# Kernel tuning notes

Measured on AMD Instinct MI355X. Metric: run time of the kernel, lower is better.

## Reference

```python
import jax, jax.numpy as jnp
import numpy as np

DIM = 1024
G = 256            # group_size
QK = 128           # query_key_dim
HID = 2048         # int(dim * expansion_factor)
NUM_BUCKETS = 32
MAX_DIST = 128
BIAS_SCALE = QK ** 0.5
LN_EPS = 1e-5


def t5_rel_bias(rel_table):
    # causal T5 relative position bias for a [G, G] block
    pos = jnp.arange(G)
    rel = pos[None, :] - pos[:, None]          # k_pos - q_pos
    n = jnp.maximum(-rel, 0)                   # causal clamp
    max_exact = NUM_BUCKETS // 2               # 16
    is_small = n < max_exact
    ln_ratio = np.log(MAX_DIST / max_exact)
    val_large = max_exact + (
        jnp.log(jnp.maximum(n, 1).astype(jnp.float32) / max_exact) / ln_ratio
        * (NUM_BUCKETS - max_exact)
    ).astype(jnp.int32)
    val_large = jnp.minimum(val_large, NUM_BUCKETS - 1)
    bucket = jnp.where(is_small, n, val_large)
    return rel_table[bucket] * BIAS_SCALE      # [G, G]


def setup_inputs() -> dict:
    key = jax.random.key(0)
    ks = jax.random.split(key, 10)
    s = 0.02
    return {
        "x": jax.random.normal(ks[0], (4, 4096, DIM), dtype=jnp.float32),
        "ln_w": jnp.ones((DIM,), jnp.float32),
        "ln_b": jnp.zeros((DIM,), jnp.float32),
        "Wh": jax.random.normal(ks[1], (DIM, 2 * HID), jnp.float32) * s,
        "bh": jnp.zeros((2 * HID,), jnp.float32),
        "Wqk": jax.random.normal(ks[2], (DIM, QK), jnp.float32) * s,
        "bqk": jnp.zeros((QK,), jnp.float32),
        "qk_w": jax.random.normal(ks[3], (4, QK), jnp.float32) * s + 1.0,
        "qk_b": jnp.zeros((4, QK), jnp.float32),
        "rel_table": jax.random.normal(ks[4], (NUM_BUCKETS,), jnp.float32) * s,
        "Wout": jax.random.normal(ks[5], (HID, DIM), jnp.float32) * s,
        "bout": jnp.zeros((DIM,), jnp.float32),
    }


def reference(x, ln_w, ln_b, Wh, bh, Wqk, bqk, qk_w, qk_b, rel_table, Wout, bout):
    b, n, _ = x.shape
    g = G
    ng = n // g

    # LayerNorm
    mu = jnp.mean(x, -1, keepdims=True)
    var = jnp.var(x, -1, keepdims=True)
    normed = (x - mu) * jax.lax.rsqrt(var + LN_EPS) * ln_w + ln_b

    # projections
    hv = jax.nn.silu(normed @ Wh + bh)
    v, gate = jnp.split(hv, 2, axis=-1)                 # [b, n, HID] each
    qk = jax.nn.silu(normed @ Wqk + bqk)                # [b, n, QK]

    # offset-scale into 4 heads
    qk4 = qk[..., None, :] * qk_w + qk_b                # [b, n, 4, QK]
    quad_q, lin_q, quad_k, lin_k = [qk4[..., h, :] for h in range(4)]

    # group: b (g n) d -> b g n d
    grp = lambda t: t.reshape(b, ng, g, t.shape[-1])
    quad_q, quad_k, lin_q, lin_k, vg = map(grp, (quad_q, quad_k, lin_q, lin_k, v))

    # quadratic branch: ReLU^2 attention with T5 bias, causal within group
    sim = jnp.einsum('bgid,bgjd->bgij', quad_q, quad_k) / g
    sim = sim + t5_rel_bias(rel_table)
    attn = jnp.square(jax.nn.relu(sim))
    causal_mask = jnp.triu(jnp.ones((g, g), bool), 1)
    attn = jnp.where(causal_mask, 0.0, attn)
    quad_out = jnp.einsum('bgij,bgje->bgie', attn, vg)  # [b, ng, g, HID]

    # linear branch: per-group kv summary, causal via shifted cumsum over groups
    lin_kv = jnp.einsum('bgnd,bgne->bgde', lin_k, vg) / g   # [b, ng, QK, HID]
    lin_kv = jnp.cumsum(lin_kv, axis=1)
    lin_kv = jnp.pad(lin_kv, ((0, 0), (1, 0), (0, 0), (0, 0)))[:, :-1]
    lin_out = jnp.einsum('bgde,bgnd->bgne', lin_kv, lin_q)  # [b, ng, g, HID]

    out = gate * (quad_out + lin_out).reshape(b, n, HID)
    return out @ Wout + bout + x
```

## Files before the change

### kernel.cpp

```cpp
#include <hip/hip_runtime.h>
#include <hip/hip_bf16.h>

typedef unsigned short u16;
typedef short s8v __attribute__((ext_vector_type(8)));
typedef float f4v __attribute__((ext_vector_type(4)));

__device__ __forceinline__ float b2f(u16 u) { return __uint_as_float(((unsigned)u) << 16); }
__device__ __forceinline__ u16 f2b(float f) {
    unsigned u = __float_as_uint(f);
    unsigned r = 0x7FFFu + ((u >> 16) & 1u);
    return (u16)((u + r) >> 16);
}
__device__ __forceinline__ float silu_f(float x) { return x / (1.0f + expf(-x)); }

__device__ __forceinline__ void gld16(const u16* g, u16* l) {
    __builtin_amdgcn_global_load_lds((const __attribute__((address_space(1))) unsigned*)g,
                                     (__attribute__((address_space(3))) unsigned*)l, 16, 0, 0);
}

__device__ __forceinline__ void mfma_block(const u16* Al, const u16* Bl, f4v acc[4][4],
                                           int wr, int wc, int l15, int quad, int l7) {
#pragma unroll
    for (int ks = 0; ks < 2; ++ks) {
        s8v af[4], bf[4];
        int cch = ((ks * 4 + quad) ^ l7) * 8;
#pragma unroll
        for (int mi = 0; mi < 4; ++mi)
            af[mi] = *(const s8v*)(Al + (wr * 64 + mi * 16 + l15) * 64 + cch);
#pragma unroll
        for (int ni = 0; ni < 4; ++ni)
            bf[ni] = *(const s8v*)(Bl + (wc * 64 + ni * 16 + l15) * 64 + cch);
#pragma unroll
        for (int mi = 0; mi < 4; ++mi)
#pragma unroll
            for (int ni = 0; ni < 4; ++ni)
                acc[mi][ni] = __builtin_amdgcn_mfma_f32_16x16x32_bf16(af[mi], bf[ni], acc[mi][ni], 0, 0, 0);
    }
}


__device__ __forceinline__ void stage_half(const u16* __restrict__ src, int K, int kbase,
                                           u16* dst, int t) {
    const int row = t >> 2, ch = t & 3;
    const int csw = (ch ^ (row & 3) ^ ((row >> 2) & 3)) * 8;
    gld16(src + (size_t)row * K + kbase + csw, dst + row * 32 + ch * 8);
    gld16(src + (size_t)(row + 128) * K + kbase + csw, dst + (row + 128) * 32 + ch * 8);
}

__device__ __forceinline__ void readA4(const u16* Ab, s8v af[4], int rbase, int l15, int quad) {
#pragma unroll
    for (int mi = 0; mi < 4; ++mi) {
        int ra = rbase + mi * 16 + l15;
        af[mi] = *(const s8v*)(Ab + ra * 32 + ((quad ^ (ra & 3) ^ ((ra >> 2) & 3)) * 8));
    }
}

__device__ __forceinline__ void kloop256(const u16* __restrict__ Ag, const u16* __restrict__ Bg,
                                         int K, int NT, u16* lds8, f4v (&acc)[8][4],
                                         int t, int wm, int wn, int l15, int quad) {
#pragma unroll
    for (int T = 0; T < 3; ++T) {
        u16* Ab = lds8 + T * 16384;
        stage_half(Ag, K, T * 32, Ab, t);
        stage_half(Bg, K, T * 32, Ab + 8192, t);
    }
    asm volatile("s_waitcnt vmcnt(8)" ::: "memory");
    __builtin_amdgcn_s_barrier();

    s8v bf[4];
    for (int T = 0; T < NT; ++T) {
        const u16* Ab = lds8 + (T & 3) * 16384;
        const u16* Bb = Ab + 8192;
        u16* Sb = lds8 + ((T + 3) & 3) * 16384;
        const bool st = (T < NT - 3);
        s8v af[4];
#pragma unroll
        for (int ni = 0; ni < 4; ++ni) {
            int rb = wn * 64 + ni * 16 + l15;
            bf[ni] = *(const s8v*)(Bb + rb * 32 + ((quad ^ (rb & 3) ^ ((rb >> 2) & 3)) * 8));
        }
        readA4(Ab, af, wm * 128, l15, quad);
        if (st) stage_half(Ag, K, (T + 3) * 32, Sb, t);
        __builtin_amdgcn_s_setprio(1);
#pragma unroll
        for (int mi = 0; mi < 4; ++mi)
#pragma unroll
            for (int ni = 0; ni < 4; ++ni)
                acc[mi][ni] = __builtin_amdgcn_mfma_f32_16x16x32_bf16(af[mi], bf[ni], acc[mi][ni], 0, 0, 0);
        __builtin_amdgcn_s_setprio(0);
        __builtin_amdgcn_s_barrier();
        readA4(Ab, af, wm * 128 + 64, l15, quad);
        if (st) stage_half(Bg, K, (T + 3) * 32, Sb + 8192, t);
        __builtin_amdgcn_s_setprio(1);
#pragma unroll
        for (int mi = 0; mi < 4; ++mi)
#pragma unroll
            for (int ni = 0; ni < 4; ++ni)
                acc[4 + mi][ni] = __builtin_amdgcn_mfma_f32_16x16x32_bf16(af[mi], bf[ni], acc[4 + mi][ni], 0, 0, 0);
        __builtin_amdgcn_s_setprio(0);
        if (T < NT - 3)       asm volatile("s_waitcnt vmcnt(8)" ::: "memory");
        else if (T == NT - 3) asm volatile("s_waitcnt vmcnt(4)" ::: "memory");
        else if (T == NT - 2) asm volatile("s_waitcnt vmcnt(0)" ::: "memory");
        __builtin_amdgcn_s_barrier();
    }
}


__global__ __launch_bounds__(256) void convT_kernel(const float* __restrict__ in,
                                                    u16* __restrict__ out, int K, int N) {
    __shared__ float tile[32][33];
    int k0 = blockIdx.y * 32, n0 = blockIdx.x * 32;
    int t = threadIdx.x;
    int r = t >> 5, c = t & 31;
#pragma unroll
    for (int rr = r; rr < 32; rr += 8) tile[rr][c] = in[(size_t)(k0 + rr) * N + n0 + c];
    __syncthreads();
#pragma unroll
    for (int rr = r; rr < 32; rr += 8) out[(size_t)(n0 + rr) * K + k0 + c] = f2b(tile[c][rr]);
}

__global__ __launch_bounds__(256) void ln_kernel(const float* __restrict__ x,
                                                 const float* __restrict__ w,
                                                 const float* __restrict__ bsh,
                                                 u16* __restrict__ out) {
    int row = blockIdx.x, t = threadIdx.x;
    const float* xr = x + (size_t)row * 1024;
    float4 u = *reinterpret_cast<const float4*>(xr + t * 4);
    float s = u.x + u.y + u.z + u.w;
    float s2 = u.x * u.x + u.y * u.y + u.z * u.z + u.w * u.w;
#pragma unroll
    for (int o = 32; o; o >>= 1) {
        s += __shfl_down(s, o, 64);
        s2 += __shfl_down(s2, o, 64);
    }
    __shared__ float rs[4], rs2[4];
    int wid = t >> 6;
    if ((t & 63) == 0) { rs[wid] = s; rs2[wid] = s2; }
    __syncthreads();
    float S = rs[0] + rs[1] + rs[2] + rs[3];
    float S2 = rs2[0] + rs2[1] + rs2[2] + rs2[3];
    float mu = S * (1.0f / 1024.0f);
    float var = S2 * (1.0f / 1024.0f) - mu * mu;
    float rinv = rsqrtf(var + 1e-5f);
    float4 uw = *reinterpret_cast<const float4*>(w + t * 4);
    float4 ub = *reinterpret_cast<const float4*>(bsh + t * 4);
    ushort4 o;
    o.x = f2b((u.x - mu) * rinv * uw.x + ub.x);
    o.y = f2b((u.y - mu) * rinv * uw.y + ub.y);
    o.z = f2b((u.z - mu) * rinv * uw.z + ub.z);
    o.w = f2b((u.w - mu) * rinv * uw.w + ub.w);
    *reinterpret_cast<ushort4*>(out + (size_t)row * 1024 + t * 4) = o;
}

__global__ __launch_bounds__(512) void gemm_hv256(const u16* __restrict__ A,
                                                  const u16* __restrict__ Bt,
                                                  const float* __restrict__ bias,
                                                  u16* __restrict__ vT,
                                                  u16* __restrict__ gate) {
    __shared__ __align__(16) u16 lds8[65536];
    const int t = threadIdx.x;
    const int lane = t & 63, w = t >> 6;
    const int wm = w >> 2, wn = w & 3;
    const int l15 = lane & 15, quad = lane >> 4;

    int wg = blockIdx.x;
    wg = (wg & 7) * 128 + (wg >> 3);
    const int by = wg >> 4, bx = wg & 15;
    const int m0 = by * 256, n0 = bx * 256;

    f4v acc[8][4] = {};
    kloop256(A + (size_t)m0 * 1024, Bt + (size_t)n0 * 1024, 1024, 32,
             lds8, acc, t, wm, wn, l15, quad);

    const bool isV = (n0 < 2048);
    const int bg = by;
#pragma unroll
    for (int ni = 0; ni < 4; ++ni) {
        int n = n0 + wn * 64 + ni * 16 + l15;
        float bs = bias[n];
#pragma unroll
        for (int mi = 0; mi < 8; ++mi) {
            int mloc = wm * 128 + mi * 16 + quad * 4;
            if (isV) {
                ushort4 o;
                o.x = f2b(silu_f(acc[mi][ni][0] + bs));
                o.y = f2b(silu_f(acc[mi][ni][1] + bs));
                o.z = f2b(silu_f(acc[mi][ni][2] + bs));
                o.w = f2b(silu_f(acc[mi][ni][3] + bs));
                *reinterpret_cast<ushort4*>(vT + ((size_t)bg * 2048 + n) * 256 + mloc) = o;
            } else {
#pragma unroll
                for (int reg = 0; reg < 4; ++reg)
                    gate[(size_t)(m0 + mloc + reg) * 2048 + (n - 2048)] =
                        f2b(silu_f(acc[mi][ni][reg] + bs));
            }
        }
    }
}

__global__ __launch_bounds__(512) void gemm_out256(const u16* __restrict__ A,
                                                   const u16* __restrict__ Bt,
                                                   const float* __restrict__ bias,
                                                   const float* __restrict__ resid,
                                                   float* __restrict__ C) {
    __shared__ __align__(16) u16 lds8[65536];
    const int t = threadIdx.x;
    const int lane = t & 63, w = t >> 6;
    const int wm = w >> 2, wn = w & 3;
    const int l15 = lane & 15, quad = lane >> 4;

    int wg = blockIdx.x;
    wg = (wg & 7) * 32 + (wg >> 3);
    const int by = wg >> 2, bx = wg & 3;
    const int m0 = by * 256, n0 = bx * 256;

    f4v acc[8][4] = {};
    kloop256(A + (size_t)m0 * 2048, Bt + (size_t)n0 * 2048, 2048, 64,
             lds8, acc, t, wm, wn, l15, quad);

#pragma unroll
    for (int ni = 0; ni < 4; ++ni) {
        int n = n0 + wn * 64 + ni * 16 + l15;
        float bs = bias[n];
#pragma unroll
        for (int mi = 0; mi < 8; ++mi) {
#pragma unroll
            for (int reg = 0; reg < 4; ++reg) {
                int m = m0 + wm * 128 + mi * 16 + quad * 4 + reg;
                C[(size_t)m * 1024 + n] = acc[mi][ni][reg] + bs + resid[(size_t)m * 1024 + n];
            }
        }
    }
}

__global__ __launch_bounds__(256) void gemm_qk(const u16* __restrict__ A,
                                               const u16* __restrict__ Bt,
                                               const float* __restrict__ bias,
                                               u16* __restrict__ C) {
    __shared__ __align__(16) u16 Al[128 * 64];
    __shared__ __align__(16) u16 Bl[128 * 64];
    const int t = threadIdx.x;
    const int lane = t & 63, w = t >> 6;
    const int wr = w >> 1, wc = w & 1;
    const int l15 = lane & 15, quad = lane >> 4, l7 = lane & 7;
    const int m0 = blockIdx.y * 128;
    const int sr = t >> 3, ss = t & 7;

    f4v acc[4][4] = {};
    for (int k0 = 0; k0 < 1024; k0 += 64) {
#pragma unroll
        for (int i = 0; i < 4; ++i) {
            int r = i * 32 + sr;
            int q = ss ^ (r & 7);
            gld16(A + (size_t)(m0 + r) * 1024 + q * 8 + k0, Al + i * 2048 + t * 8);
            gld16(Bt + (size_t)r * 1024 + q * 8 + k0, Bl + i * 2048 + t * 8);
        }
        __syncthreads();
        mfma_block(Al, Bl, acc, wr, wc, l15, quad, l7);
        __syncthreads();
    }
#pragma unroll
    for (int ni = 0; ni < 4; ++ni) {
        int n = wc * 64 + ni * 16 + l15;
        float bs = bias[n];
#pragma unroll
        for (int mi = 0; mi < 4; ++mi) {
#pragma unroll
            for (int reg = 0; reg < 4; ++reg) {
                int m = m0 + wr * 64 + mi * 16 + quad * 4 + reg;
                C[(size_t)m * 128 + n] = f2b(silu_f(acc[mi][ni][reg] + bs));
            }
        }
    }
}

__global__ __launch_bounds__(256) void klT_kernel(const u16* __restrict__ qk,
                                                  const float* __restrict__ qk_w,
                                                  const float* __restrict__ qk_b,
                                                  u16* __restrict__ klT) {
    __shared__ __align__(16) u16 tile[64][128];
    const int bg = blockIdx.x >> 2, jc = (blockIdx.x & 3) * 64;
    const int t = threadIdx.x;
    const int r = t >> 4, c = (t & 15) * 8;
#pragma unroll
    for (int rr = 0; rr < 64; rr += 16)
        *(s8v*)(&tile[r + rr][c]) =
            *(const s8v*)(qk + (size_t)(bg * 256 + jc + r + rr) * 128 + c);
    __syncthreads();
    const int d = t & 127, jb = (t >> 7) * 32;
    const float kw = qk_w[3 * 128 + d], kb = qk_b[3 * 128 + d];
    s8v ov[4];
#pragma unroll
    for (int q = 0; q < 4; ++q)
#pragma unroll
        for (int j = 0; j < 8; ++j)
            ov[q][j] = (short)f2b(b2f(tile[jb + q * 8 + j][d]) * kw + kb);
    u16* dst = klT + ((size_t)bg * 128 + d) * 256 + jc + jb;
#pragma unroll
    for (int q = 0; q < 4; ++q) *(s8v*)(dst + q * 8) = ov[q];
}

__global__ __launch_bounds__(256) void scores_kernel(const u16* __restrict__ qk,
                                                     const float* __restrict__ qk_w,
                                                     const float* __restrict__ qk_b,
                                                     const float* __restrict__ rel_table,
                                                     u16* __restrict__ Sbuf) {
    __shared__ __align__(16) u16 qkl[256 * 128];
    __shared__ float biasn[256];
    __shared__ float w0[128], b0[128], w1[128], b1[128], w2[128], b2v[128];
    const int t = threadIdx.x;
    const int bg = blockIdx.x >> 1, mt = blockIdx.x & 1;
    const int lane = t & 63, w = t >> 6;
    const int wr = w >> 1, wc = w & 1;
    const int l15 = lane & 15, quad = lane >> 4;

    if (t < 128) {
        w0[t] = qk_w[t];        b0[t] = qk_b[t];
        w1[t] = qk_w[128 + t];  b1[t] = qk_b[128 + t];
        w2[t] = qk_w[256 + t];  b2v[t] = qk_b[256 + t];
    }
    {
        int n = t;
        int bucket;
        if (n < 16) bucket = n;
        else {
            float v = logf((float)n / 16.0f) / 2.0794415416798357f * 16.0f;
            int vl = 16 + (int)v;
            bucket = vl > 31 ? 31 : vl;
        }
        biasn[n] = rel_table[bucket] * 11.313708498984761f;
    }
#pragma unroll
    for (int it = 0; it < 16; ++it) {
        int r = (t >> 4) + it * 16, c = (t & 15) * 8;
        *(s8v*)(qkl + r * 128 + c) = *(const s8v*)(qk + ((size_t)(bg * 256 + r)) * 128 + c);
    }
    __syncthreads();

    f4v acc[4][8] = {};
#pragma unroll
    for (int kstep = 0; kstep < 4; ++kstep) {
        int kc = kstep * 32 + quad * 8;
        float w0f[8], b0f[8], w2f[8], b2f_[8];
#pragma unroll
        for (int j = 0; j < 8; ++j) {
            w0f[j] = w0[kc + j]; b0f[j] = b0[kc + j];
            w2f[j] = w2[kc + j]; b2f_[j] = b2v[kc + j];
        }
        s8v af[4];
#pragma unroll
        for (int mi = 0; mi < 4; ++mi) {
            int ra = mt * 128 + wr * 64 + mi * 16 + l15;
            s8v raw = *(const s8v*)(qkl + ra * 128 + kc);
#pragma unroll
            for (int j = 0; j < 8; ++j) af[mi][j] = (short)f2b(b2f((u16)raw[j]) * w0f[j] + b0f[j]);
        }
#pragma unroll
        for (int np = 0; np < 2; ++np) {
            s8v bf[4];
#pragma unroll
            for (int ni = 0; ni < 4; ++ni) {
                int rb = wc * 128 + (np * 4 + ni) * 16 + l15;
                s8v raw = *(const s8v*)(qkl + rb * 128 + kc);
#pragma unroll
                for (int j = 0; j < 8; ++j) bf[ni][j] = (short)f2b(b2f((u16)raw[j]) * w2f[j] + b2f_[j]);
            }
#pragma unroll
            for (int mi = 0; mi < 4; ++mi)
#pragma unroll
                for (int ni = 0; ni < 4; ++ni)
                    acc[mi][np * 4 + ni] = __builtin_amdgcn_mfma_f32_16x16x32_bf16(af[mi], bf[ni], acc[mi][np * 4 + ni], 0, 0, 0);
        }
    }
#pragma unroll
    for (int ni = 0; ni < 8; ++ni) {
        int gj = wc * 128 + ni * 16 + l15;
#pragma unroll
        for (int mi = 0; mi < 4; ++mi) {
#pragma unroll
            for (int reg = 0; reg < 4; ++reg) {
                int gi = mt * 128 + wr * 64 + mi * 16 + quad * 4 + reg;
                float aval = 0.0f;
                if (gj <= gi) {
                    float sv = acc[mi][ni][reg] * (1.0f / 256.0f) + biasn[gi - gj];
                    sv = fmaxf(sv, 0.0f);
                    aval = sv * sv;
                }
                Sbuf[((size_t)bg * 256 + gi) * 384 + gj] = f2b(aval);
            }
        }
    }
#pragma unroll
    for (int it = 0; it < 8; ++it) {
        int i = mt * 128 + (t >> 4) + it * 16;
        int d = (t & 15) * 8;
        s8v raw = *(const s8v*)(qkl + i * 128 + d);
        u16* dst = Sbuf + ((size_t)bg * 256 + i) * 384 + 256 + d;
#pragma unroll
        for (int j = 0; j < 8; ++j)
            dst[j] = f2b(b2f((u16)raw[j]) * w1[d + j] + b1[d + j]);
    }
}

__global__ __launch_bounds__(256) void kv_gemm(const u16* __restrict__ vT,
                                               const u16* __restrict__ klT,
                                               u16* __restrict__ kvT) {
    __shared__ __align__(16) u16 Al[128 * 64];
    __shared__ __align__(16) u16 Bl[128 * 64];
    const int t = threadIdx.x;
    const int lane = t & 63, w = t >> 6;
    const int wr = w >> 1, wc = w & 1;
    const int l15 = lane & 15, quad = lane >> 4, l7 = lane & 7;
    const int bg = blockIdx.y, m0 = blockIdx.x * 128;
    const int sr = t >> 3, ss = t & 7;

    const u16* Av = vT + (size_t)bg * 2048 * 256;
    const u16* Bk = klT + (size_t)bg * 128 * 256;

    f4v acc[4][4] = {};
    for (int k0 = 0; k0 < 256; k0 += 64) {
#pragma unroll
        for (int i = 0; i < 4; ++i) {
            int r = i * 32 + sr;
            int q = ss ^ (r & 7);
            gld16(Av + (size_t)(m0 + r) * 256 + q * 8 + k0, Al + i * 2048 + t * 8);
            gld16(Bk + (size_t)r * 256 + q * 8 + k0, Bl + i * 2048 + t * 8);
        }
        __syncthreads();
        mfma_block(Al, Bl, acc, wr, wc, l15, quad, l7);
        __syncthreads();
    }
#pragma unroll
    for (int ni = 0; ni < 4; ++ni) {
        int n = wc * 64 + ni * 16 + l15;
#pragma unroll
        for (int mi = 0; mi < 4; ++mi) {
#pragma unroll
            for (int reg = 0; reg < 4; ++reg) {
                int m = m0 + wr * 64 + mi * 16 + quad * 4 + reg;
                kvT[((size_t)bg * 2048 + m) * 128 + n] = f2b(acc[mi][ni][reg] * (1.0f / 256.0f));
            }
        }
    }
}

__global__ __launch_bounds__(256) void prefix_kernel(u16* __restrict__ kvT) {
    size_t tid = (size_t)blockIdx.x * 256 + threadIdx.x;
    int d = (int)(tid & 127);
    int e = (int)((tid >> 7) & 2047);
    int b = (int)(tid >> 18);
    size_t base = ((size_t)(b * 16) * 2048 + e) * 128 + d;
    const size_t gs = 2048 * 128;
    float vals[16];
#pragma unroll
    for (int g = 0; g < 16; ++g) vals[g] = b2f(kvT[base + (size_t)g * gs]);
    float s = 0.0f;
#pragma unroll
    for (int g = 0; g < 16; ++g) {
        kvT[base + (size_t)g * gs] = f2b(s);
        s += vals[g];
    }
}

__global__ __launch_bounds__(256) void attn_gemm(const u16* __restrict__ Sbuf,
                                                 const u16* __restrict__ vT,
                                                 const u16* __restrict__ kvT,
                                                 u16* __restrict__ gate) {
    __shared__ __align__(16) u16 Al[128 * 64];
    __shared__ __align__(16) u16 Bl[128 * 64];
    const int t = threadIdx.x;
    const int lane = t & 63, w = t >> 6;
    const int wr = w >> 1, wc = w & 1;
    const int l15 = lane & 15, quad = lane >> 4, l7 = lane & 7;
    const int bg = blockIdx.y >> 1, mt = blockIdx.y & 1;
    const int n0 = blockIdx.x * 128;
    const int sr = t >> 3, ss = t & 7;

    const u16* Abase = Sbuf + ((size_t)bg * 256 + mt * 128) * 384;
    const u16* Bv = vT + (size_t)bg * 2048 * 256;
    const u16* Bk = kvT + (size_t)bg * 2048 * 128;

    f4v acc[4][4] = {};
    for (int k0 = 0; k0 < 256; k0 += 64) {
#pragma unroll
        for (int i = 0; i < 4; ++i) {
            int r = i * 32 + sr;
            int q = ss ^ (r & 7);
            gld16(Abase + (size_t)r * 384 + q * 8 + k0, Al + i * 2048 + t * 8);
            gld16(Bv + (size_t)(n0 + r) * 256 + q * 8 + k0, Bl + i * 2048 + t * 8);
        }
        __syncthreads();
        mfma_block(Al, Bl, acc, wr, wc, l15, quad, l7);
        __syncthreads();
    }
    for (int k0 = 0; k0 < 128; k0 += 64) {
#pragma unroll
        for (int i = 0; i < 4; ++i) {
            int r = i * 32 + sr;
            int q = ss ^ (r & 7);
            gld16(Abase + (size_t)r * 384 + 256 + q * 8 + k0, Al + i * 2048 + t * 8);
            gld16(Bk + (size_t)(n0 + r) * 128 + q * 8 + k0, Bl + i * 2048 + t * 8);
        }
        __syncthreads();
        mfma_block(Al, Bl, acc, wr, wc, l15, quad, l7);
        __syncthreads();
    }
#pragma unroll
    for (int ni = 0; ni < 4; ++ni) {
        int e = n0 + wc * 64 + ni * 16 + l15;
#pragma unroll
        for (int mi = 0; mi < 4; ++mi) {
#pragma unroll
            for (int reg = 0; reg < 4; ++reg) {
                int gi = mt * 128 + wr * 64 + mi * 16 + quad * 4 + reg;
                u16* p = gate + ((size_t)bg * 256 + gi) * 2048 + e;
                *p = f2b(acc[mi][ni][reg] * b2f(*p));
            }
        }
    }
}

extern "C" void kernel_launch(void* const* d_in, const int* in_sizes, int n_in,
                              void* d_out, int out_size, void* d_ws, size_t ws_size,
                              hipStream_t stream) {
    const float* x = (const float*)d_in[0];
    const float* ln_w = (const float*)d_in[1];
    const float* ln_b = (const float*)d_in[2];
    const float* Wh = (const float*)d_in[3];
    const float* bh = (const float*)d_in[4];
    const float* Wqk = (const float*)d_in[5];
    const float* bqk = (const float*)d_in[6];
    const float* qk_w = (const float*)d_in[7];
    const float* qk_b = (const float*)d_in[8];
    const float* rel_table = (const float*)d_in[9];
    const float* Wout = (const float*)d_in[10];
    const float* bout = (const float*)d_in[11];
    float* out = (float*)d_out;

    char* ws = (char*)d_ws;
    u16* normed = (u16*)(ws);
    u16* kvT    = (u16*)(ws);
    u16* gate   = (u16*)(ws + 33554432ull);
    u16* vT     = (u16*)(ws + 100663296ull);
    u16* qk     = (u16*)(ws + 167772160ull);
    u16* WhT    = (u16*)(ws + 171966464ull);
    u16* klT    = (u16*)(ws + 171966464ull);
    u16* WoutT  = (u16*)(ws + 180355072ull);
    u16* Sbuf   = (u16*)(ws + 184549376ull);
    u16* WqkT   = (u16*)(ws + 184549376ull);

    convT_kernel<<<dim3(128, 32), 256, 0, stream>>>(Wh, WhT, 1024, 4096);
    convT_kernel<<<dim3(32, 64), 256, 0, stream>>>(Wout, WoutT, 2048, 1024);
    convT_kernel<<<dim3(4, 32), 256, 0, stream>>>(Wqk, WqkT, 1024, 128);
    ln_kernel<<<16384, 256, 0, stream>>>(x, ln_w, ln_b, normed);
    gemm_hv256<<<1024, 512, 0, stream>>>(normed, WhT, bh, vT, gate);
    gemm_qk<<<dim3(1, 128), 256, 0, stream>>>(normed, WqkT, bqk, qk);
    klT_kernel<<<256, 256, 0, stream>>>(qk, qk_w, qk_b, klT);
    scores_kernel<<<128, 256, 0, stream>>>(qk, qk_w, qk_b, rel_table, Sbuf);
    kv_gemm<<<dim3(16, 64), 256, 0, stream>>>(vT, klT, kvT);
    prefix_kernel<<<4096, 256, 0, stream>>>(kvT);
    attn_gemm<<<dim3(16, 128), 256, 0, stream>>>(Sbuf, vT, kvT, gate);
    gemm_out256<<<256, 512, 0, stream>>>(gate, WoutT, bout, x, out);
}
```

Baseline: 577.7 us.

## Restructure 256x256 GEMM k-loop into double-buffered 64-wide stages with explicit fences

Replaces the 4-slot ring of 32-wide K stages with two 64-wide buffers, each split into two K planes, processed in four MFMA phases per iteration. Each phase overlaps a global-to-LDS load for a future plane, and explicit lgkmcnt fences and scheduling barriers pin the LDS reads before the MFMAs. The aim is to halve loop-iteration overhead and get a more predictable overlap of loads with compute. In exchange it adds more s_barrier calls per K step, which can stall warps.

```diff
diff --git a/kernel.cpp b/kernel.cpp
--- a/kernel.cpp
+++ b/kernel.cpp
@@ -39,68 +39,86 @@
 }
 
 
-__device__ __forceinline__ void stage_half(const u16* __restrict__ src, int K, int kbase,
-                                           u16* dst, int t) {
-    const int row = t >> 2, ch = t & 3;
-    const int csw = (ch ^ (row & 3) ^ ((row >> 2) & 3)) * 8;
-    gld16(src + (size_t)row * K + kbase + csw, dst + row * 32 + ch * 8);
-    gld16(src + (size_t)(row + 128) * K + kbase + csw, dst + (row + 128) * 32 + ch * 8);
-}
-
-__device__ __forceinline__ void readA4(const u16* Ab, s8v af[4], int rbase, int l15, int quad) {
-#pragma unroll
-    for (int mi = 0; mi < 4; ++mi) {
-        int ra = rbase + mi * 16 + l15;
-        af[mi] = *(const s8v*)(Ab + ra * 32 + ((quad ^ (ra & 3) ^ ((ra >> 2) & 3)) * 8));
-    }
-}
-
-__device__ __forceinline__ void kloop256(const u16* __restrict__ Ag, const u16* __restrict__ Bg,
-                                         int K, int NT, u16* lds8, f4v (&acc)[8][4],
-                                         int t, int wm, int wn, int l15, int quad) {
-#pragma unroll
-    for (int T = 0; T < 3; ++T) {
-        u16* Ab = lds8 + T * 16384;
-        stage_half(Ag, K, T * 32, Ab, t);
-        stage_half(Bg, K, T * 32, Ab + 8192, t);
-    }
-    asm volatile("s_waitcnt vmcnt(8)" ::: "memory");
+__device__ __forceinline__ void stage_plane(const u16* __restrict__ src, int K, int kcol,
+                                            u16* dstPlane, int t) {
+    const int r = t >> 2, ch = t & 3;
+    const int sw = (ch ^ (r & 3) ^ ((r >> 2) & 3)) * 8;
+    gld16(src + (size_t)r * K + kcol + sw, dstPlane + t * 8);
+    gld16(src + (size_t)(r + 128) * K + kcol + sw, dstPlane + 4096 + t * 8);
+}
+
+__device__ __forceinline__ void read_frag4(const u16* plane, s8v (&f)[4], int base, int l15, int quad) {
+#pragma unroll
+    for (int i = 0; i < 4; ++i) {
+        int r = base + i * 16 + l15;
+        f[i] = *(const s8v*)(plane + r * 32 + ((quad ^ (r & 3) ^ ((r >> 2) & 3)) * 8));
+    }
+}
+
+__device__ __forceinline__ void mfma_quad(f4v (&a4)[4][4], const s8v (&af)[4], const s8v (&bf)[4]) {
+    __builtin_amdgcn_s_setprio(1);
+#pragma unroll
+    for (int mi = 0; mi < 4; ++mi)
+#pragma unroll
+        for (int ni = 0; ni < 4; ++ni)
+            a4[mi][ni] = __builtin_amdgcn_mfma_f32_16x16x32_bf16(af[mi], bf[ni], a4[mi][ni], 0, 0, 0);
+    __builtin_amdgcn_s_setprio(0);
+}
+
+#define LGKM0_FENCE() do { \
+    asm volatile("s_waitcnt lgkmcnt(0)" ::: "memory"); \
+    __builtin_amdgcn_sched_barrier(0); } while (0)
+
+__device__ __forceinline__ void kloop8(const u16* __restrict__ Ag, const u16* __restrict__ Bg,
+                                       int K, int NT, u16* lds, f4v (&acc)[2][4][4],
+                                       int t, int wm, int wn, int l15, int quad) {
+    stage_plane(Ag, K, 0,  lds, t);
+    stage_plane(Bg, K, 0,  lds + 16384, t);
+    stage_plane(Ag, K, 32, lds + 8192, t);
+    stage_plane(Bg, K, 32, lds + 24576, t);
+    stage_plane(Ag, K, 64, lds + 32768, t);
+    stage_plane(Bg, K, 64, lds + 32768 + 16384, t);
+    asm volatile("s_waitcnt vmcnt(4)" ::: "memory");
     __builtin_amdgcn_s_barrier();
 
-    s8v bf[4];
-    for (int T = 0; T < NT; ++T) {
-        const u16* Ab = lds8 + (T & 3) * 16384;
-        const u16* Bb = Ab + 8192;
-        u16* Sb = lds8 + ((T + 3) & 3) * 16384;
-        const bool st = (T < NT - 3);
-        s8v af[4];
-#pragma unroll
-        for (int ni = 0; ni < 4; ++ni) {
-            int rb = wn * 64 + ni * 16 + l15;
-            bf[ni] = *(const s8v*)(Bb + rb * 32 + ((quad ^ (rb & 3) ^ ((rb >> 2) & 3)) * 8));
-        }
-        readA4(Ab, af, wm * 128, l15, quad);
-        if (st) stage_half(Ag, K, (T + 3) * 32, Sb, t);
-        __builtin_amdgcn_s_setprio(1);
-#pragma unroll
-        for (int mi = 0; mi < 4; ++mi)
-#pragma unroll
-            for (int ni = 0; ni < 4; ++ni)
-                acc[mi][ni] = __builtin_amdgcn_mfma_f32_16x16x32_bf16(af[mi], bf[ni], acc[mi][ni], 0, 0, 0);
-        __builtin_amdgcn_s_setprio(0);
-        __builtin_amdgcn_s_barrier();
-        readA4(Ab, af, wm * 128 + 64, l15, quad);
-        if (st) stage_half(Bg, K, (T + 3) * 32, Sb + 8192, t);
-        __builtin_amdgcn_s_setprio(1);
-#pragma unroll
-        for (int mi = 0; mi < 4; ++mi)
-#pragma unroll
-            for (int ni = 0; ni < 4; ++ni)
-                acc[4 + mi][ni] = __builtin_amdgcn_mfma_f32_16x16x32_bf16(af[mi], bf[ni], acc[4 + mi][ni], 0, 0, 0);
-        __builtin_amdgcn_s_setprio(0);
-        if (T < NT - 3)       asm volatile("s_waitcnt vmcnt(8)" ::: "memory");
-        else if (T == NT - 3) asm volatile("s_waitcnt vmcnt(4)" ::: "memory");
-        else if (T == NT - 2) asm volatile("s_waitcnt vmcnt(0)" ::: "memory");
+    const int ab0 = wm * 128, ab1 = wm * 128 + 64, bb = wn * 64;
+    s8v af[4], bf[4];
+    for (int j = 0; j < NT; ++j) {
+        u16* cur = lds + (j & 1) * 32768;
+        u16* nxt = lds + ((j + 1) & 1) * 32768;
+        const u16* Ak0 = cur;
+        const u16* Ak1 = cur + 8192;
+        const u16* Bk0 = cur + 16384;
+        const u16* Bk1 = cur + 24576;
+        const bool s1 = (j + 1 < NT), s2 = (j + 2 < NT);
+
+        read_frag4(Bk0, bf, bb, l15, quad);
+        read_frag4(Ak0, af, ab0, l15, quad);
+        if (s1) stage_plane(Ag, K, (j + 1) * 64 + 32, nxt + 8192, t);
+        __builtin_amdgcn_s_barrier();
+        LGKM0_FENCE();
+        mfma_quad(acc[0], af, bf);
+        __builtin_amdgcn_s_barrier();
+        read_frag4(Ak0, af, ab1, l15, quad);
+        if (s1) stage_plane(Bg, K, (j + 1) * 64 + 32, nxt + 24576, t);
+        __builtin_amdgcn_s_barrier();
+        LGKM0_FENCE();
+        mfma_quad(acc[1], af, bf);
+        __builtin_amdgcn_s_barrier();
+        read_frag4(Bk1, bf, bb, l15, quad);
+        read_frag4(Ak1, af, ab0, l15, quad);
+        if (s2) stage_plane(Ag, K, (j + 2) * 64, cur, t);
+        __builtin_amdgcn_s_barrier();
+        LGKM0_FENCE();
+        mfma_quad(acc[0], af, bf);
+        __builtin_amdgcn_s_barrier();
+        read_frag4(Ak1, af, ab1, l15, quad);
+        if (s2) stage_plane(Bg, K, (j + 2) * 64, cur + 16384, t);
+        if (j < NT - 2) asm volatile("s_waitcnt vmcnt(4)" ::: "memory");
+        else            asm volatile("s_waitcnt vmcnt(0)" ::: "memory");
+        __builtin_amdgcn_s_barrier();
+        LGKM0_FENCE();
+        mfma_quad(acc[1], af, bf);
         __builtin_amdgcn_s_barrier();
     }
 }
@@ -168,9 +186,9 @@
     const int by = wg >> 4, bx = wg & 15;
     const int m0 = by * 256, n0 = bx * 256;
 
-    f4v acc[8][4] = {};
-    kloop256(A + (size_t)m0 * 1024, Bt + (size_t)n0 * 1024, 1024, 32,
-             lds8, acc, t, wm, wn, l15, quad);
+    f4v acc[2][4][4] = {};
+    kloop8(A + (size_t)m0 * 1024, Bt + (size_t)n0 * 1024, 1024, 16,
+           lds8, acc, t, wm, wn, l15, quad);
 
     const bool isV = (n0 < 2048);
     const int bg = by;
@@ -179,20 +197,23 @@
         int n = n0 + wn * 64 + ni * 16 + l15;
         float bs = bias[n];
 #pragma unroll
-        for (int mi = 0; mi < 8; ++mi) {
-            int mloc = wm * 128 + mi * 16 + quad * 4;
-            if (isV) {
-                ushort4 o;
-                o.x = f2b(silu_f(acc[mi][ni][0] + bs));
-                o.y = f2b(silu_f(acc[mi][ni][1] + bs));
-                o.z = f2b(silu_f(acc[mi][ni][2] + bs));
-                o.w = f2b(silu_f(acc[mi][ni][3] + bs));
-                *reinterpret_cast<ushort4*>(vT + ((size_t)bg * 2048 + n) * 256 + mloc) = o;
-            } else {
-#pragma unroll
-                for (int reg = 0; reg < 4; ++reg)
-                    gate[(size_t)(m0 + mloc + reg) * 2048 + (n - 2048)] =
-                        f2b(silu_f(acc[mi][ni][reg] + bs));
+        for (int mg = 0; mg < 2; ++mg) {
+#pragma unroll
+            for (int m = 0; m < 4; ++m) {
+                int mloc = wm * 128 + (mg * 4 + m) * 16 + quad * 4;
+                if (isV) {
+                    ushort4 o;
+                    o.x = f2b(silu_f(acc[mg][m][ni][0] + bs));
+                    o.y = f2b(silu_f(acc[mg][m][ni][1] + bs));
+                    o.z = f2b(silu_f(acc[mg][m][ni][2] + bs));
+                    o.w = f2b(silu_f(acc[mg][m][ni][3] + bs));
+                    *reinterpret_cast<ushort4*>(vT + ((size_t)bg * 2048 + n) * 256 + mloc) = o;
+                } else {
+#pragma unroll
+                    for (int reg = 0; reg < 4; ++reg)
+                        gate[(size_t)(m0 + mloc + reg) * 2048 + (n - 2048)] =
+                            f2b(silu_f(acc[mg][m][ni][reg] + bs));
+                }
             }
         }
     }
@@ -214,20 +235,23 @@
     const int by = wg >> 2, bx = wg & 3;
     const int m0 = by * 256, n0 = bx * 256;
 
-    f4v acc[8][4] = {};
-    kloop256(A + (size_t)m0 * 2048, Bt + (size_t)n0 * 2048, 2048, 64,
-             lds8, acc, t, wm, wn, l15, quad);
+    f4v acc[2][4][4] = {};
+    kloop8(A + (size_t)m0 * 2048, Bt + (size_t)n0 * 2048, 2048, 32,
+           lds8, acc, t, wm, wn, l15, quad);
 
 #pragma unroll
     for (int ni = 0; ni < 4; ++ni) {
         int n = n0 + wn * 64 + ni * 16 + l15;
         float bs = bias[n];
 #pragma unroll
-        for (int mi = 0; mi < 8; ++mi) {
-#pragma unroll
-            for (int reg = 0; reg < 4; ++reg) {
-                int m = m0 + wm * 128 + mi * 16 + quad * 4 + reg;
-                C[(size_t)m * 1024 + n] = acc[mi][ni][reg] + bs + resid[(size_t)m * 1024 + n];
+        for (int mg = 0; mg < 2; ++mg) {
+#pragma unroll
+            for (int m = 0; m < 4; ++m) {
+#pragma unroll
+                for (int reg = 0; reg < 4; ++reg) {
+                    int mm = m0 + wm * 128 + (mg * 4 + m) * 16 + quad * 4 + reg;
+                    C[(size_t)mm * 1024 + n] = acc[mg][m][ni][reg] + bs + resid[(size_t)mm * 1024 + n];
+                }
             }
         }
     }
```

New measurement: 749.5 us. +29.7%, slower.

## Switch GEMM k-loop from 4-stage to 2-stage LDS pipeline for higher occupancy

Applied to the files above, without the earlier changes.

Replaces the four-buffer, three-ahead prefetch pipeline in the shared GEMM k-loop with a simple double buffer that loads the next tile at the start of each iteration and waits for all loads at the end. LDS per block drops from 128KB to 64KB and launch bounds request more waves per SIMD, aiming to fit more blocks per CU and hide latency through occupancy. The trade-off is a shallower prefetch depth, a full vmcnt(0) wait every iteration, and the loss of the interleaved half-staging. The extra launch-bounds requirement may also force register spills given the 8x4 accumulator tile.

```diff
diff --git a/kernel.cpp b/kernel.cpp
--- a/kernel.cpp
+++ b/kernel.cpp
@@ -56,51 +56,41 @@
 }
 
 __device__ __forceinline__ void kloop256(const u16* __restrict__ Ag, const u16* __restrict__ Bg,
-                                         int K, int NT, u16* lds8, f4v (&acc)[8][4],
+                                         int K, int NT, u16* lds, f4v (&acc)[8][4],
                                          int t, int wm, int wn, int l15, int quad) {
-#pragma unroll
-    for (int T = 0; T < 3; ++T) {
-        u16* Ab = lds8 + T * 16384;
-        stage_half(Ag, K, T * 32, Ab, t);
-        stage_half(Bg, K, T * 32, Ab + 8192, t);
-    }
-    asm volatile("s_waitcnt vmcnt(8)" ::: "memory");
+    stage_half(Ag, K, 0, lds, t);
+    stage_half(Bg, K, 0, lds + 8192, t);
+    asm volatile("s_waitcnt vmcnt(0)" ::: "memory");
     __builtin_amdgcn_s_barrier();
 
-    s8v bf[4];
     for (int T = 0; T < NT; ++T) {
-        const u16* Ab = lds8 + (T & 3) * 16384;
+        const u16* Ab = lds + (T & 1) * 16384;
         const u16* Bb = Ab + 8192;
-        u16* Sb = lds8 + ((T + 3) & 3) * 16384;
-        const bool st = (T < NT - 3);
-        s8v af[4];
+        u16* nxt = lds + ((T + 1) & 1) * 16384;
+        if (T + 1 < NT) {
+            stage_half(Ag, K, (T + 1) * 32, nxt, t);
+            stage_half(Bg, K, (T + 1) * 32, nxt + 8192, t);
+        }
+        s8v bf[4];
 #pragma unroll
         for (int ni = 0; ni < 4; ++ni) {
             int rb = wn * 64 + ni * 16 + l15;
             bf[ni] = *(const s8v*)(Bb + rb * 32 + ((quad ^ (rb & 3) ^ ((rb >> 2) & 3)) * 8));
         }
-        readA4(Ab, af, wm * 128, l15, quad);
-        if (st) stage_half(Ag, K, (T + 3) * 32, Sb, t);
-        __builtin_amdgcn_s_setprio(1);
-#pragma unroll
-        for (int mi = 0; mi < 4; ++mi)
-#pragma unroll
-            for (int ni = 0; ni < 4; ++ni)
-                acc[mi][ni] = __builtin_amdgcn_mfma_f32_16x16x32_bf16(af[mi], bf[ni], acc[mi][ni], 0, 0, 0);
-        __builtin_amdgcn_s_setprio(0);
-        __builtin_amdgcn_s_barrier();
-        readA4(Ab, af, wm * 128 + 64, l15, quad);
-        if (st) stage_half(Bg, K, (T + 3) * 32, Sb + 8192, t);
-        __builtin_amdgcn_s_setprio(1);
-#pragma unroll
-        for (int mi = 0; mi < 4; ++mi)
-#pragma unroll
-            for (int ni = 0; ni < 4; ++ni)
-                acc[4 + mi][ni] = __builtin_amdgcn_mfma_f32_16x16x32_bf16(af[mi], bf[ni], acc[4 + mi][ni], 0, 0, 0);
-        __builtin_amdgcn_s_setprio(0);
-        if (T < NT - 3)       asm volatile("s_waitcnt vmcnt(8)" ::: "memory");
-        else if (T == NT - 3) asm volatile("s_waitcnt vmcnt(4)" ::: "memory");
-        else if (T == NT - 2) asm volatile("s_waitcnt vmcnt(0)" ::: "memory");
+#pragma unroll
+        for (int mg = 0; mg < 2; ++mg) {
+            s8v af[4];
+            readA4(Ab, af, wm * 128 + mg * 64, l15, quad);
+            __builtin_amdgcn_s_setprio(1);
+#pragma unroll
+            for (int mi = 0; mi < 4; ++mi)
+#pragma unroll
+                for (int ni = 0; ni < 4; ++ni)
+                    acc[mg * 4 + mi][ni] =
+                        __builtin_amdgcn_mfma_f32_16x16x32_bf16(af[mi], bf[ni], acc[mg * 4 + mi][ni], 0, 0, 0);
+            __builtin_amdgcn_s_setprio(0);
+        }
+        asm volatile("s_waitcnt vmcnt(0)" ::: "memory");
         __builtin_amdgcn_s_barrier();
     }
 }
@@ -152,12 +142,12 @@
     *reinterpret_cast<ushort4*>(out + (size_t)row * 1024 + t * 4) = o;
 }
 
-__global__ __launch_bounds__(512) void gemm_hv256(const u16* __restrict__ A,
-                                                  const u16* __restrict__ Bt,
-                                                  const float* __restrict__ bias,
-                                                  u16* __restrict__ vT,
-                                                  u16* __restrict__ gate) {
-    __shared__ __align__(16) u16 lds8[65536];
+__global__ __launch_bounds__(512, 4) void gemm_hv256(const u16* __restrict__ A,
+                                                     const u16* __restrict__ Bt,
+                                                     const float* __restrict__ bias,
+                                                     u16* __restrict__ vT,
+                                                     u16* __restrict__ gate) {
+    __shared__ __align__(16) u16 lds8[32768];
     const int t = threadIdx.x;
     const int lane = t & 63, w = t >> 6;
     const int wm = w >> 2, wn = w & 3;
@@ -198,12 +188,12 @@
     }
 }
 
-__global__ __launch_bounds__(512) void gemm_out256(const u16* __restrict__ A,
-                                                   const u16* __restrict__ Bt,
-                                                   const float* __restrict__ bias,
-                                                   const float* __restrict__ resid,
-                                                   float* __restrict__ C) {
-    __shared__ __align__(16) u16 lds8[65536];
+__global__ __launch_bounds__(512, 4) void gemm_out256(const u16* __restrict__ A,
+                                                      const u16* __restrict__ Bt,
+                                                      const float* __restrict__ bias,
+                                                      const float* __restrict__ resid,
+                                                      float* __restrict__ C) {
+    __shared__ __align__(16) u16 lds8[32768];
     const int t = threadIdx.x;
     const int lane = t & 63, w = t >> 6;
     const int wm = w >> 2, wn = w & 3;
```

Measured after the change: 1.734 ms. +200.1%, slower.
